# Performance work log

Hardware: AMD Instinct MI355X
Metric: run time of the kernel (lower is better)

## Reference

```python
import jax, jax.numpy as jnp
import numpy as np

WS = (2, 7, 7)   # window size (d, h, w)
SS = (1, 3, 3)   # shift size
EPS = 1e-5


def _rel_pos_index(ws):
    d, h, w = np.arange(ws[0]), np.arange(ws[1]), np.arange(ws[2])
    coords = np.stack(np.meshgrid(d, h, w, indexing='ij'))        # (3, wd, wh, ww)
    flat = coords.reshape(3, -1)                                   # (3, N)
    rel = flat[:, :, None] - flat[:, None, :]                      # (3, N, N)
    rel = rel.transpose(1, 2, 0).astype(np.int64)                  # (N, N, 3)
    rel[:, :, 0] += ws[0] - 1
    rel[:, :, 1] += ws[1] - 1
    rel[:, :, 2] += ws[2] - 1
    rel[:, :, 0] *= (2 * ws[1] - 1) * (2 * ws[2] - 1)
    rel[:, :, 1] *= 2 * ws[2] - 1
    return rel.sum(-1)                                             # (N, N)


def _window_partition(x, ws):
    B, D, H, W, C = x.shape
    x = x.reshape(B, D // ws[0], ws[0], H // ws[1], ws[1], W // ws[2], ws[2], C)
    return x.transpose(0, 1, 3, 5, 2, 4, 6, 7).reshape(-1, ws[0] * ws[1] * ws[2], C)


def _window_reverse(win, ws, B, D, H, W):
    x = win.reshape(B, D // ws[0], H // ws[1], W // ws[2], ws[0], ws[1], ws[2], -1)
    return x.transpose(0, 1, 4, 2, 5, 3, 6, 7).reshape(B, D, H, W, -1)


def _attn_mask(D, H, W, ws, ss):
    img = np.zeros((1, D, H, W, 1), np.float32)
    cnt = 0
    for dsl in (slice(None, -ws[0]), slice(-ws[0], -ss[0]), slice(-ss[0], None)):
        for hsl in (slice(None, -ws[1]), slice(-ws[1], -ss[1]), slice(-ss[1], None)):
            for wsl in (slice(None, -ws[2]), slice(-ws[2], -ss[2]), slice(-ss[2], None)):
                img[:, dsl, hsl, wsl, :] = cnt
                cnt += 1
    mw = _window_partition(img, ws)[..., 0]                        # (nW, N)
    am = mw[:, None, :] - mw[:, :, None]                           # (nW, N, N)
    return np.where(am != 0, np.float32(-100.0), np.float32(0.0))


def _ln(x, g, b):
    m = x.mean(-1, keepdims=True)
    v = ((x - m) ** 2).mean(-1, keepdims=True)
    return (x - m) / jnp.sqrt(v + EPS) * g + b


def setup_inputs():
    key = jax.random.key(0)
    B, D, H, W, C = 2, 8, 56, 56, 256
    nH, hidden = 8, 1024
    ks = jax.random.split(key, 8)
    s = 0.02
    inp = {
        'x': jax.random.normal(ks[0], (B, D, H, W, C), jnp.float32),
        'qkv_w': jax.random.normal(ks[1], (3 * C, C), jnp.float32) * s,
        'qkv_b': jnp.zeros((3 * C,), jnp.float32),
        'proj_w': jax.random.normal(ks[2], (C, C), jnp.float32) * s,
        'proj_b': jnp.zeros((C,), jnp.float32),
        'rpb_table': jax.random.normal(ks[3], (3 * 13 * 13, nH), jnp.float32) * s,
        'ln1_g': jnp.ones((C,), jnp.float32),
        'ln1_b': jnp.zeros((C,), jnp.float32),
        'ln2_g': jnp.ones((C,), jnp.float32),
        'ln2_b': jnp.zeros((C,), jnp.float32),
        'fc1_w': jax.random.normal(ks[4], (hidden, C), jnp.float32) * s,
        'fc1_b': jnp.zeros((hidden,), jnp.float32),
        'fc2_w': jax.random.normal(ks[5], (C, hidden), jnp.float32) * s,
        'fc2_b': jnp.zeros((C,), jnp.float32),
        'rel_idx': jnp.asarray(_rel_pos_index(WS), jnp.int32),
        'attn_mask': jnp.asarray(_attn_mask(D, H, W, WS, SS)),
        'num_heads': nH,
    }
    return inp


def reference(x, qkv_w, qkv_b, proj_w, proj_b, rpb_table, ln1_g, ln1_b, ln2_g,
              ln2_b, fc1_w, fc1_b, fc2_w, fc2_b, rel_idx, attn_mask, num_heads):
    B, D, H, W, C = x.shape
    N = WS[0] * WS[1] * WS[2]
    hd = C // num_heads
    scale = hd ** (-0.5)

    shortcut = x
    h = _ln(x, ln1_g, ln1_b)
    # cyclic shift
    h = jnp.roll(h, shift=(-SS[0], -SS[1], -SS[2]), axis=(1, 2, 3))
    win = _window_partition(h, WS)                                 # (B_, N, C)

    qkv = win @ qkv_w.T + qkv_b                                    # (B_, N, 3C)
    qkv = qkv.reshape(-1, N, 3, num_heads, hd).transpose(2, 0, 3, 1, 4)
    q, k, v = qkv[0] * scale, qkv[1], qkv[2]                       # (B_, nH, N, hd)

    attn = jnp.einsum('bhid,bhjd->bhij', q, k)                     # (B_, nH, N, N)
    bias = rpb_table[rel_idx.reshape(-1)].reshape(N, N, num_heads).transpose(2, 0, 1)
    attn = attn + bias[None]
    nW = attn_mask.shape[0]
    attn = attn.reshape(B, nW, num_heads, N, N) + attn_mask[None, :, None]
    attn = jax.nn.softmax(attn.reshape(-1, num_heads, N, N), axis=-1)

    out = jnp.einsum('bhij,bhjd->bhid', attn, v)                   # (B_, nH, N, hd)
    out = out.transpose(0, 2, 1, 3).reshape(-1, N, C)
    out = out @ proj_w.T + proj_b

    xr = _window_reverse(out, WS, B, D, H, W)
    xr = jnp.roll(xr, shift=SS, axis=(1, 2, 3))                    # reverse shift
    x = shortcut + xr

    h2 = _ln(x, ln2_g, ln2_b)
    m = jax.nn.gelu(h2 @ fc1_w.T + fc1_b, approximate=False)
    m = m @ fc2_w.T + fc2_b
    return x + m
```

## Files before the change

kernel.cpp:

```cpp
#include <hip/hip_runtime.h>
#include <hip/hip_bf16.h>
#include <math.h>

#define B_  2
#define D_  8
#define H_  56
#define W_  56
#define C_  256
#define NH_ 8
#define HD_ 32
#define N_  98
#define NWIN_TOT 512
#define TOK (B_*D_*H_*W_)
#define HID 1024

typedef short bf16x8 __attribute__((ext_vector_type(8)));
typedef float f32x4  __attribute__((ext_vector_type(4)));

__device__ __forceinline__ ushort f2b(float f) {
    union { float f; unsigned u; } v; v.f = f;
    unsigned r = v.u + 0x7fff + ((v.u >> 16) & 1);
    return (ushort)(r >> 16);
}
__device__ __forceinline__ float b2f(ushort h) {
    union { unsigned u; float f; } v; v.u = ((unsigned)h) << 16;
    return v.f;
}

__device__ __forceinline__ void glds16(const void* gsrc, void* lds_dst) {
    __builtin_amdgcn_global_load_lds(
        (const __attribute__((address_space(1))) unsigned int*)gsrc,
        (__attribute__((address_space(3))) unsigned int*)lds_dst,
        16, 0, 0);
}

__device__ __forceinline__ int tok_of_winrow(int r) {
    int wid  = r / N_;
    int n    = r - wid * N_;
    int b    = wid >> 8;
    int rem  = wid & 255;
    int di   = rem >> 6;
    int hi   = (rem >> 3) & 7;
    int wi   = rem & 7;
    int wd   = n / 49;
    int rem2 = n - wd * 49;
    int wh   = rem2 / 7;
    int ww   = rem2 - wh * 7;
    int d = di * 2 + wd + 1; if (d >= D_) d -= D_;
    int h = hi * 7 + wh + 3; if (h >= H_) h -= H_;
    int w = wi * 7 + ww + 3; if (w >= W_) w -= W_;
    return ((b * D_ + d) * H_ + h) * W_ + w;
}

__device__ __forceinline__ float gelu_exact(float x) {
    return 0.5f * x * (1.0f + erff(x * 0.70710678118654752f));
}

template<bool GATHER>
__global__ __launch_bounds__(256)
void ln_kernel(const float* __restrict__ x, const float* __restrict__ g,
               const float* __restrict__ bta, ushort* __restrict__ out, int nrows) {
    int wave = blockIdx.x * 4 + (threadIdx.x >> 6);
    int lane = threadIdx.x & 63;
    if (wave >= nrows) return;
    int srow = GATHER ? tok_of_winrow(wave) : wave;
    float4 v = ((const float4*)(x + (size_t)srow * C_))[lane];
    float s  = v.x + v.y + v.z + v.w;
    float ss = v.x*v.x + v.y*v.y + v.z*v.z + v.w*v.w;
    #pragma unroll
    for (int o = 32; o; o >>= 1) { s += __shfl_xor(s, o); ss += __shfl_xor(ss, o); }
    float mean = s * (1.0f / C_);
    float var  = ss * (1.0f / C_) - mean * mean;
    float rstd = rsqrtf(var + 1e-5f);
    float4 gg = ((const float4*)g)[lane];
    float4 bb = ((const float4*)bta)[lane];
    ushort4 o4;
    o4.x = f2b((v.x - mean) * rstd * gg.x + bb.x);
    o4.y = f2b((v.y - mean) * rstd * gg.y + bb.y);
    o4.z = f2b((v.z - mean) * rstd * gg.z + bb.z);
    o4.w = f2b((v.w - mean) * rstd * gg.w + bb.w);
    ((ushort4*)(out + (size_t)wave * C_))[lane] = o4;
}

__global__ void tbl_kernel(const int* __restrict__ rel_idx,
                           const float* __restrict__ rpb,
                           const float* __restrict__ mask,
                           ushort* __restrict__ Tb) {
    int idx = blockIdx.x * blockDim.x + threadIdx.x;
    if (idx >= 64 * N_ * N_) return;
    int ph = idx / (N_ * N_);
    int ij = idx - ph * (N_ * N_);
    int p = ph >> 3, hh = ph & 7;
    int di = (p & 1) ? 3 : 0, hi = (p & 2) ? 7 : 0, wi = (p & 4) ? 7 : 0;
    int rep = di * 64 + hi * 8 + wi;
    float b = rpb[rel_idx[ij] * NH_ + hh];
    float m = mask[(size_t)rep * (N_ * N_) + ij];
    Tb[(size_t)ph * (N_ * N_) + ij] = f2b(b + m);
}

__global__ void f2b_kernel(const float* __restrict__ src, ushort* __restrict__ dst, int n) {
    int i = (blockIdx.x * blockDim.x + threadIdx.x) * 4;
    if (i >= n) return;
    float4 v = *(const float4*)(src + i);
    ushort4 o; o.x = f2b(v.x); o.y = f2b(v.y); o.z = f2b(v.z); o.w = f2b(v.w);
    *(ushort4*)(dst + i) = o;
}

template<int MODE>
__global__ __launch_bounds__(256)
void gemm_bf16(const ushort* __restrict__ A, const ushort* __restrict__ Wm,
               const float* __restrict__ bias, void* __restrict__ Cout,
               const void* __restrict__ resid, int M, int K, int Nout) {
    __shared__ __align__(16) char lds[32768];
    char* ldsA = lds;
    char* ldsB = lds + 16384;
    const int tid  = threadIdx.x;
    const int wv   = tid >> 6, lane = tid & 63;
    const int m0   = blockIdx.x * 128, n0 = blockIdx.y * 128;
    const int wrow = (wv >> 1) * 64, wcol = (wv & 1) * 64;
    const int lr8  = lane >> 3, lc = lane & 7;

    f32x4 acc[4][4] = {};

    const ushort* Ag[4]; const ushort* Bg[4];
    #pragma unroll
    for (int i = 0; i < 4; ++i) {
        int row = (wv * 4 + i) * 8 + lr8;
        int gc  = lc ^ (row & 7);
        Ag[i] = A  + (size_t)(m0 + row) * K + gc * 8;
        Bg[i] = Wm + (size_t)(n0 + row) * K + gc * 8;
    }

    for (int k0 = 0; k0 < K; k0 += 64) {
        #pragma unroll
        for (int i = 0; i < 4; ++i) {
            glds16(Ag[i] + k0, ldsA + (wv * 4 + i) * 1024);
            glds16(Bg[i] + k0, ldsB + (wv * 4 + i) * 1024);
        }
        __syncthreads();
        #pragma unroll
        for (int kk = 0; kk < 2; ++kk) {
            bf16x8 af[4], bfr[4];
            #pragma unroll
            for (int i = 0; i < 4; ++i) {
                int r = wrow + i * 16 + (lane & 15);
                int c = (lane >> 4) + kk * 4;
                af[i]  = *(const bf16x8*)(ldsA + r * 128 + ((c ^ (r & 7)) * 16));
                int r2 = wcol + i * 16 + (lane & 15);
                bfr[i] = *(const bf16x8*)(ldsB + r2 * 128 + ((c ^ (r2 & 7)) * 16));
            }
            #pragma unroll
            for (int i = 0; i < 4; ++i)
                #pragma unroll
                for (int j = 0; j < 4; ++j)
                    acc[i][j] = __builtin_amdgcn_mfma_f32_16x16x32_bf16(af[i], bfr[j], acc[i][j], 0, 0, 0);
        }
        __syncthreads();
    }

    int colg[4]; float bv[4];
    #pragma unroll
    for (int j = 0; j < 4; ++j) {
        colg[j] = n0 + wcol + j * 16 + (lane & 15);
        bv[j]   = bias[colg[j]];
    }
    #pragma unroll
    for (int i = 0; i < 4; ++i) {
        #pragma unroll
        for (int r = 0; r < 4; ++r) {
            int rowg = m0 + wrow + i * 16 + ((lane >> 4) << 2) + r;
            int tok = (MODE == 1) ? tok_of_winrow(rowg) : rowg;
            #pragma unroll
            for (int j = 0; j < 4; ++j) {
                float v = acc[i][j][r] + bv[j];
                if (MODE == 0) {
                    ((ushort*)Cout)[(size_t)rowg * Nout + colg[j]] = f2b(v);
                } else if (MODE == 1) {
                    v += ((const float*)resid)[(size_t)tok * C_ + colg[j]];
                    ((float*)Cout)[(size_t)tok * C_ + colg[j]] = v;
                } else if (MODE == 2) {
                    ((ushort*)Cout)[(size_t)rowg * Nout + colg[j]] = f2b(gelu_exact(v));
                } else {
                    v += ((const float*)resid)[(size_t)rowg * Nout + colg[j]];
                    ((float*)Cout)[(size_t)rowg * Nout + colg[j]] = v;
                }
            }
        }
    }
}

#define QOFF 0
#define KOFF 7168
#define VOFF 14336
#define POFF 22528
#define SMEM_BYTES 39936
__global__ __launch_bounds__(256)
void attn_mfma(const ushort* __restrict__ qkv, const ushort* __restrict__ Tb,
               ushort* __restrict__ attn_out) {
    __shared__ __align__(16) char smem[SMEM_BYTES];
    ushort (*Pl)[16][136] = (ushort (*)[16][136])(smem + POFF);
    const int b    = blockIdx.x;
    const int wid  = (b & 7) + ((b >> 6) << 3);
    const int hh   = (b >> 3) & 7;
    const int tid  = threadIdx.x;
    const int wv   = tid >> 6, lane = tid & 63;
    const int lrow = lane & 15, lgrp = lane >> 4;
    const float scale = 0.17677669529663687f;

    const ushort* base = qkv + (size_t)wid * N_ * 768 + hh * 32;
    const int rem = wid & 255;
    const int pat = (((rem >> 6) == 3) ? 1 : 0) | ((((rem >> 3) & 7) == 7) ? 2 : 0)
                  | (((rem & 7) == 7) ? 4 : 0);
    const ushort* tb = Tb + (size_t)(pat * 8 + hh) * (N_ * N_);

    {
        uint4 z = {0, 0, 0, 0};
        uint4* l4 = (uint4*)(smem + 21504);
        for (int i = tid; i < (SMEM_BYTES - 21504) / 16; i += 256) l4[i] = z;
    }
    __syncthreads();

    #pragma unroll
    for (int sect = 0; sect < 3; ++sect) {
        char* dstbase = smem + sect * 7168;
        const ushort* src = base + sect * 256;
        for (int c0 = wv * 64; c0 < 448; c0 += 256) {
            int c = c0 + lane;
            int r = c >> 2; if (r > 97) r = 97;
            int cc = c & 3;
            glds16(src + (size_t)r * 768 + ((cc ^ (r & 3)) * 8), dstbase + c0 * 16);
        }
    }
    __syncthreads();

    const int swz = (lgrp ^ (lrow & 3)) << 4;

    bf16x8 kf[7];
    #pragma unroll
    for (int nj = 0; nj < 7; ++nj)
        kf[nj] = *(const bf16x8*)(smem + KOFF + (nj * 16 + lrow) * 64 + swz);

    bf16x8 vf[2][4];
    #pragma unroll
    for (int dt = 0; dt < 2; ++dt)
        #pragma unroll
        for (int kt = 0; kt < 4; ++kt) {
            bf16x8 tmp;
            #pragma unroll
            for (int t = 0; t < 8; ++t) {
                int R = kt * 32 + lgrp * 8 + t;
                int q = dt * 2 + (lrow >> 3);
                tmp[t] = *(const short*)(smem + VOFF + R * 64 +
                                         ((q ^ (t & 3)) << 4) + ((lrow & 7) << 1));
            }
            vf[dt][kt] = tmp;
        }

    for (int mi = wv; mi < 7; mi += 4) {
        const int ibase = mi * 16;
        bf16x8 qf = *(const bf16x8*)(smem + QOFF + (ibase + lrow) * 64 + swz);

        f32x4 s[7];
        #pragma unroll
        for (int nj = 0; nj < 7; ++nj) {
            f32x4 z = {0.f, 0.f, 0.f, 0.f};
            s[nj] = __builtin_amdgcn_mfma_f32_16x16x32_bf16(qf, kf[nj], z, 0, 0, 0);
        }

        #pragma unroll
        for (int nj = 0; nj < 7; ++nj) {
            int j = nj * 16 + lrow;
            #pragma unroll
            for (int r = 0; r < 4; ++r) {
                int i = ibase + lgrp * 4 + r;
                s[nj][r] = (j < N_ && i < N_)
                    ? s[nj][r] * scale + b2f(tb[i * N_ + j]) : -1e30f;
            }
        }

        float rinv[4];
        #pragma unroll
        for (int r = 0; r < 4; ++r) {
            float acc = 0.f;
            #pragma unroll
            for (int nj = 0; nj < 7; ++nj) {
                float p = __expf(s[nj][r]);
                s[nj][r] = p;
                acc += p;
            }
            #pragma unroll
            for (int o = 1; o < 16; o <<= 1) acc += __shfl_xor(acc, o);
            rinv[r] = 1.f / acc;
        }

        #pragma unroll
        for (int nj = 0; nj < 7; ++nj)
            #pragma unroll
            for (int r = 0; r < 4; ++r)
                Pl[wv][lgrp * 4 + r][nj * 16 + lrow] = f2b(s[nj][r] * rinv[r]);

        f32x4 o0 = {0.f, 0.f, 0.f, 0.f}, o1 = {0.f, 0.f, 0.f, 0.f};
        #pragma unroll
        for (int kt = 0; kt < 4; ++kt) {
            bf16x8 pf = *(const bf16x8*)(&Pl[wv][lrow][kt * 32 + lgrp * 8]);
            o0 = __builtin_amdgcn_mfma_f32_16x16x32_bf16(pf, vf[0][kt], o0, 0, 0, 0);
            o1 = __builtin_amdgcn_mfma_f32_16x16x32_bf16(pf, vf[1][kt], o1, 0, 0, 0);
        }

        #pragma unroll
        for (int r = 0; r < 4; ++r) {
            int i = ibase + lgrp * 4 + r;
            if (i < N_) {
                size_t rb = ((size_t)(wid * N_ + i)) * C_ + hh * 32;
                attn_out[rb + lrow]      = f2b(o0[r]);
                attn_out[rb + 16 + lrow] = f2b(o1[r]);
            }
        }
    }
}

extern "C" void kernel_launch(void* const* d_in, const int* in_sizes, int n_in,
                              void* d_out, int out_size, void* d_ws, size_t ws_size,
                              hipStream_t stream) {
    const float* x      = (const float*)d_in[0];
    const float* qkv_w  = (const float*)d_in[1];
    const float* qkv_b  = (const float*)d_in[2];
    const float* proj_w = (const float*)d_in[3];
    const float* proj_b = (const float*)d_in[4];
    const float* rpb    = (const float*)d_in[5];
    const float* ln1_g  = (const float*)d_in[6];
    const float* ln1_b  = (const float*)d_in[7];
    const float* ln2_g  = (const float*)d_in[8];
    const float* ln2_b  = (const float*)d_in[9];
    const float* fc1_w  = (const float*)d_in[10];
    const float* fc1_b  = (const float*)d_in[11];
    const float* fc2_w  = (const float*)d_in[12];
    const float* fc2_b  = (const float*)d_in[13];
    const int*   rel_idx= (const int*)d_in[14];
    const float* mask   = (const float*)d_in[15];
    float* out = (float*)d_out;

    char* ws = (char*)d_ws;
    ushort* regionA = (ushort*)ws;
    ushort* regionB = (ushort*)(ws + (size_t)TOK * HID * 2);
    ushort* wq  = (ushort*)(ws + (size_t)TOK * HID * 2 + (size_t)TOK * C_ * 2);
    ushort* wp  = wq + 768 * 256;
    ushort* w1  = wp + 256 * 256;
    ushort* w2  = w1 + HID * 256;
    ushort* Tb  = w2 + 256 * HID;

    tbl_kernel<<<(64 * N_ * N_ + 255) / 256, 256, 0, stream>>>(rel_idx, rpb, mask, Tb);
    f2b_kernel<<<(768 * 256 / 4 + 255) / 256, 256, 0, stream>>>(qkv_w, wq, 768 * 256);
    f2b_kernel<<<(256 * 256 / 4 + 255) / 256, 256, 0, stream>>>(proj_w, wp, 256 * 256);
    f2b_kernel<<<(HID * 256 / 4 + 255) / 256, 256, 0, stream>>>(fc1_w, w1, HID * 256);
    f2b_kernel<<<(256 * HID / 4 + 255) / 256, 256, 0, stream>>>(fc2_w, w2, 256 * HID);

    ln_kernel<true><<<TOK / 4, 256, 0, stream>>>(x, ln1_g, ln1_b, regionB, TOK);

    {
        dim3 g(TOK / 128, 768 / 128);
        gemm_bf16<0><<<g, 256, 0, stream>>>(regionB, wq, qkv_b, regionA, nullptr, TOK, 256, 768);
    }

    attn_mfma<<<NWIN_TOT * NH_, 256, 0, stream>>>(regionA, Tb, regionB);

    {
        dim3 g(TOK / 128, 256 / 128);
        gemm_bf16<1><<<g, 256, 0, stream>>>(regionB, wp, proj_b, out, x, TOK, 256, 256);
    }

    ln_kernel<false><<<TOK / 4, 256, 0, stream>>>(out, ln2_g, ln2_b, regionB, TOK);

    {
        dim3 g(TOK / 128, HID / 128);
        gemm_bf16<2><<<g, 256, 0, stream>>>(regionB, w1, fc1_b, regionA, nullptr, TOK, 256, HID);
    }

    {
        dim3 g(TOK / 128, 256 / 128);
        gemm_bf16<3><<<g, 256, 0, stream>>>(regionA, w2, fc2_b, out, out, TOK, HID, 256);
    }
}
```

Before: 293.3 us.

## Pre-swizzle bias/mask table into MFMA fragment layout and load Q directly

The bias+mask table is rebuilt in a per-lane, MFMA-fragment-ordered packed layout with bounds padding baked in. The attention kernel can then fetch it with coalesced 32-bit loads and no per-element index math or bounds checks. Q is read straight from global memory instead of being staged in LDS, which shrinks shared memory and may raise occupancy. The four weight-conversion launches are merged into one grid to cut launch overhead.

```diff
diff --git a/kernel.cpp b/kernel.cpp
--- a/kernel.cpp
+++ b/kernel.cpp
@@ -82,28 +82,50 @@
     ((ushort4*)(out + (size_t)wave * C_))[lane] = o4;
 }
 
+#define TB2_WORDS (8 * 8 * 7 * 14 * 64)
 __global__ void tbl_kernel(const int* __restrict__ rel_idx,
                            const float* __restrict__ rpb,
                            const float* __restrict__ mask,
-                           ushort* __restrict__ Tb) {
+                           uint* __restrict__ Tb2) {
     int idx = blockIdx.x * blockDim.x + threadIdx.x;
-    if (idx >= 64 * N_ * N_) return;
-    int ph = idx / (N_ * N_);
-    int ij = idx - ph * (N_ * N_);
-    int p = ph >> 3, hh = ph & 7;
-    int di = (p & 1) ? 3 : 0, hi = (p & 2) ? 7 : 0, wi = (p & 4) ? 7 : 0;
+    if (idx >= TB2_WORDS) return;
+    int lane = idx & 63;
+    int t    = idx >> 6;
+    int nq   = t % 14;  int t2 = t / 14;
+    int mi   = t2 % 7;  int ph = t2 / 7;
+    int pat  = ph >> 3, hh = ph & 7;
+    int nj   = nq >> 1, q = nq & 1;
+    int lrow = lane & 15, lgrp = lane >> 4;
+    int j  = nj * 16 + lrow;
+    int i0 = mi * 16 + lgrp * 4 + q * 2;
+    int di = (pat & 1) ? 3 : 0, hi = (pat & 2) ? 7 : 0, wi = (pat & 4) ? 7 : 0;
     int rep = di * 64 + hi * 8 + wi;
-    float b = rpb[rel_idx[ij] * NH_ + hh];
-    float m = mask[(size_t)rep * (N_ * N_) + ij];
-    Tb[(size_t)ph * (N_ * N_) + ij] = f2b(b + m);
-}
-
-__global__ void f2b_kernel(const float* __restrict__ src, ushort* __restrict__ dst, int n) {
+    float lo = -1e30f, hv = -1e30f;
+    if (j < N_) {
+        if (i0 < N_)
+            lo = rpb[rel_idx[i0 * N_ + j] * NH_ + hh] + mask[(size_t)rep * (N_*N_) + i0 * N_ + j];
+        if (i0 + 1 < N_)
+            hv = rpb[rel_idx[(i0+1) * N_ + j] * NH_ + hh] + mask[(size_t)rep * (N_*N_) + (i0+1) * N_ + j];
+    }
+    Tb2[idx] = (uint)f2b(lo) | ((uint)f2b(hv) << 16);
+}
+
+__global__ void f2b4_kernel(const float* __restrict__ s0, ushort* __restrict__ d0, int n0,
+                            const float* __restrict__ s1, ushort* __restrict__ d1, int n1,
+                            const float* __restrict__ s2, ushort* __restrict__ d2, int n2,
+                            const float* __restrict__ s3, ushort* __restrict__ d3, int n3) {
+    const float* s; ushort* d; int n;
+    switch (blockIdx.y) {
+        case 0: s = s0; d = d0; n = n0; break;
+        case 1: s = s1; d = d1; n = n1; break;
+        case 2: s = s2; d = d2; n = n2; break;
+        default: s = s3; d = d3; n = n3; break;
+    }
     int i = (blockIdx.x * blockDim.x + threadIdx.x) * 4;
     if (i >= n) return;
-    float4 v = *(const float4*)(src + i);
+    float4 v = *(const float4*)(s + i);
     ushort4 o; o.x = f2b(v.x); o.y = f2b(v.y); o.z = f2b(v.z); o.w = f2b(v.w);
-    *(ushort4*)(dst + i) = o;
+    *(ushort4*)(d + i) = o;
 }
 
 template<int MODE>
@@ -189,13 +211,12 @@
     }
 }
 
-#define QOFF 0
-#define KOFF 7168
-#define VOFF 14336
-#define POFF 22528
-#define SMEM_BYTES 39936
+#define KOFF 0
+#define VOFF 7168
+#define POFF 15360
+#define SMEM_BYTES 32768
 __global__ __launch_bounds__(256)
-void attn_mfma(const ushort* __restrict__ qkv, const ushort* __restrict__ Tb,
+void attn_mfma(const ushort* __restrict__ qkv, const uint* __restrict__ Tb2,
                ushort* __restrict__ attn_out) {
     __shared__ __align__(16) char smem[SMEM_BYTES];
     ushort (*Pl)[16][136] = (ushort (*)[16][136])(smem + POFF);
@@ -211,24 +232,23 @@
     const int rem = wid & 255;
     const int pat = (((rem >> 6) == 3) ? 1 : 0) | ((((rem >> 3) & 7) == 7) ? 2 : 0)
                   | (((rem & 7) == 7) ? 4 : 0);
-    const ushort* tb = Tb + (size_t)(pat * 8 + hh) * (N_ * N_);
+    const uint* tb2 = Tb2 + (size_t)((pat * 8 + hh) * 7) * 14 * 64 + lane;
 
     {
         uint4 z = {0, 0, 0, 0};
-        uint4* l4 = (uint4*)(smem + 21504);
-        for (int i = tid; i < (SMEM_BYTES - 21504) / 16; i += 256) l4[i] = z;
+        uint4* l4 = (uint4*)(smem + 14336);
+        for (int i = tid; i < (SMEM_BYTES - 14336) / 16; i += 256) l4[i] = z;
     }
     __syncthreads();
 
     #pragma unroll
-    for (int sect = 0; sect < 3; ++sect) {
+    for (int sect = 0; sect < 2; ++sect) {
         char* dstbase = smem + sect * 7168;
-        const ushort* src = base + sect * 256;
-        for (int c0 = wv * 64; c0 < 448; c0 += 256) {
-            int c = c0 + lane;
+        const ushort* src = base + 256 + sect * 256;
+        for (int c = tid; c < 448; c += 256) {
             int r = c >> 2; if (r > 97) r = 97;
             int cc = c & 3;
-            glds16(src + (size_t)r * 768 + ((cc ^ (r & 3)) * 8), dstbase + c0 * 16);
+            glds16(src + (size_t)r * 768 + ((cc ^ (r & 3)) * 8), dstbase + c * 16);
         }
     }
     __syncthreads();
@@ -258,7 +278,13 @@
 
     for (int mi = wv; mi < 7; mi += 4) {
         const int ibase = mi * 16;
-        bf16x8 qf = *(const bf16x8*)(smem + QOFF + (ibase + lrow) * 64 + swz);
+
+        uint tw[14];
+        const uint* tbm = tb2 + mi * 14 * 64;
+        #pragma unroll
+        for (int u = 0; u < 14; ++u) tw[u] = tbm[u * 64];
+
+        bf16x8 qf = *(const bf16x8*)(base + (size_t)(ibase + lrow) * 768 + lgrp * 8);
 
         f32x4 s[7];
         #pragma unroll
@@ -269,12 +295,11 @@
 
         #pragma unroll
         for (int nj = 0; nj < 7; ++nj) {
-            int j = nj * 16 + lrow;
             #pragma unroll
             for (int r = 0; r < 4; ++r) {
-                int i = ibase + lgrp * 4 + r;
-                s[nj][r] = (j < N_ && i < N_)
-                    ? s[nj][r] * scale + b2f(tb[i * N_ + j]) : -1e30f;
+                uint w = tw[nj * 2 + (r >> 1)];
+                ushort hb = (r & 1) ? (ushort)(w >> 16) : (ushort)(w & 0xffff);
+                s[nj][r] = s[nj][r] * scale + b2f(hb);
             }
         }
 
@@ -347,13 +372,16 @@
     ushort* wp  = wq + 768 * 256;
     ushort* w1  = wp + 256 * 256;
     ushort* w2  = w1 + HID * 256;
-    ushort* Tb  = w2 + 256 * HID;
-
-    tbl_kernel<<<(64 * N_ * N_ + 255) / 256, 256, 0, stream>>>(rel_idx, rpb, mask, Tb);
-    f2b_kernel<<<(768 * 256 / 4 + 255) / 256, 256, 0, stream>>>(qkv_w, wq, 768 * 256);
-    f2b_kernel<<<(256 * 256 / 4 + 255) / 256, 256, 0, stream>>>(proj_w, wp, 256 * 256);
-    f2b_kernel<<<(HID * 256 / 4 + 255) / 256, 256, 0, stream>>>(fc1_w, w1, HID * 256);
-    f2b_kernel<<<(256 * HID / 4 + 255) / 256, 256, 0, stream>>>(fc2_w, w2, 256 * HID);
+    uint*   Tb2 = (uint*)(w2 + 256 * HID);
+
+    tbl_kernel<<<(TB2_WORDS + 255) / 256, 256, 0, stream>>>(rel_idx, rpb, mask, Tb2);
+    {
+        dim3 g(256, 4);
+        f2b4_kernel<<<g, 256, 0, stream>>>(qkv_w, wq, 768 * 256,
+                                           proj_w, wp, 256 * 256,
+                                           fc1_w, w1, HID * 256,
+                                           fc2_w, w2, 256 * HID);
+    }
 
     ln_kernel<true><<<TOK / 4, 256, 0, stream>>>(x, ln1_g, ln1_b, regionB, TOK);
 
@@ -362,7 +390,7 @@
         gemm_bf16<0><<<g, 256, 0, stream>>>(regionB, wq, qkv_b, regionA, nullptr, TOK, 256, 768);
     }
 
-    attn_mfma<<<NWIN_TOT * NH_, 256, 0, stream>>>(regionA, Tb, regionB);
+    attn_mfma<<<NWIN_TOT * NH_, 256, 0, stream>>>(regionA, Tb2, regionB);
 
     {
         dim3 g(TOK / 128, 256 / 128);
```

Measured after the change: 258.2 us, median of 2. 1.14x faster.
